# Kernel tuning notes

Measured on AMD Instinct MI355X. Metric: run time of the kernel, lower is better.

## Reference

```python
import jax, jax.numpy as jnp
import numpy as np

C, H, W = 3, 2048, 2048
N_ANN = 64
P = 512  # patch resolution
RESIZE_FRAC = 0.5  # deterministic midpoint of resize_range=(0.25, 0.75)
MIN_SIZE = 10


def setup_inputs() -> dict:
    key = jax.random.key(0)
    k1, k2, k3, k4 = jax.random.split(key, 4)
    image = jax.random.normal(k1, (C, H, W), jnp.float32)
    patch = jax.random.uniform(k2, (C, P, P), jnp.float32)
    # build valid normalized xyxy boxes (x1<x2, y1<y2) inside the image
    centers = jax.random.uniform(k3, (N_ANN, 2), minval=0.2, maxval=0.8)
    sizes = jax.random.uniform(k4, (N_ANN, 2), minval=0.10, maxval=0.30)
    xy1 = jnp.clip(centers - sizes / 2, 0.0, 1.0)
    xy2 = jnp.clip(centers + sizes / 2, 0.0, 1.0)
    annotations = jnp.concatenate([xy1, xy2], axis=1).astype(jnp.float32)  # [N,4] xyxy
    return {"image": image, "annotations": annotations, "patch": patch}


def reference(image, annotations, patch):
    """MODE_CENTER_BBOX forward: for each bbox, bilinearly resize the patch to
    wh x wh (wh = min(bbox_w, bbox_h) * RESIZE_FRAC, >= MIN_SIZE), then paste it
    centered in the bbox (clamped to the image). embed_patch's mask arithmetic
    (image_mask*image + patch_mask*patch) is exactly a region overwrite."""
    c, h, w = image.shape
    # normalized_annotations=True: scale by [W, H, W, H] then floor to long
    ann = np.asarray(annotations * jnp.array([w, h, w, h], jnp.float32)).astype(np.int64)
    img = image
    for x1, y1, x2, y2 in ann:
        bw, bh = int(x2 - x1), int(y2 - y1)
        wh = max(int(min(bw, bh) * RESIZE_FRAC), MIN_SIZE)
        rp = jax.image.resize(patch, (c, wh, wh), method="bilinear")
        x = int(x1) + bw // 2 - wh // 2
        y = int(y1) + bh // 2 - wh // 2
        y = max(min(h - wh, y), 0)
        x = max(min(w - wh, x), 0)
        img = img.at[:, y:y + wh, x:x + wh].set(rp)
    return img
```

## Files before the change

kernel.cpp:

```cpp
#include <hip/hip_runtime.h>

#define CCH 3
#define HH 2048
#define WW 2048
#define NANN 64
#define PSZ 512
#define HWIMG (HH * WW)
#define PP (PSZ * PSZ)
#define WHMAX 308
#define OYB 4
#define CHS ((size_t)PSZ * WHMAX)

__global__ void prep_kernel(const float* __restrict__ ann, int* __restrict__ meta) {
    int a = threadIdx.x;
    if (a >= NANN) return;
    float x1f = ann[a * 4 + 0] * (float)WW;
    float y1f = ann[a * 4 + 1] * (float)HH;
    float x2f = ann[a * 4 + 2] * (float)WW;
    float y2f = ann[a * 4 + 3] * (float)HH;
    int x1 = (int)x1f, y1 = (int)y1f, x2 = (int)x2f, y2 = (int)y2f;
    int bw = x2 - x1, bh = y2 - y1;
    int mn = bw < bh ? bw : bh;
    int wh = mn / 2;
    if (wh < 10) wh = 10;
    int x = x1 + bw / 2 - wh / 2;
    int y = y1 + bh / 2 - wh / 2;
    y = min(HH - wh, y); y = max(y, 0);
    x = min(WW - wh, x); x = max(x, 0);
    meta[a * 4 + 0] = x;
    meta[a * 4 + 1] = y;
    meta[a * 4 + 2] = wh;
    meta[a * 4 + 3] = 0;
}

__global__ __launch_bounds__(256) void resize_y4_kernel(
    const float* __restrict__ patch, const int* __restrict__ meta,
    float* __restrict__ tmp)
{
    const int a   = blockIdx.y;
    const int oy0 = blockIdx.x * OYB;
    const int wh  = meta[a * 4 + 2];
    if (oy0 >= wh) return;

    const int xx = threadIdx.x * 2;
    const float inv = 512.0f / (float)wh;
    const float rs  = (float)wh / 512.0f;

    float syf[OYB];
#pragma unroll
    for (int i = 0; i < OYB; ++i)
        syf[i] = ((float)(oy0 + i) + 0.5f) * inv - 0.5f;

    const int ylast = min(oy0 + OYB - 1, wh - 1);
    const float syfL = ((float)ylast + 0.5f) * inv - 0.5f;
    const int ylo = max(0,       (int)ceilf(syf[0] - inv));
    const int yhi = min(PSZ - 1, (int)floorf(syfL + inv));

    float2 ac[OYB][3];
    float dy[OYB];
#pragma unroll
    for (int i = 0; i < OYB; ++i) {
        dy[i] = 0.f;
#pragma unroll
        for (int c = 0; c < 3; ++c) { ac[i][c].x = 0.f; ac[i][c].y = 0.f; }
    }

    const float* p = patch + xx;
#pragma unroll 2
    for (int yy = ylo; yy <= yhi; ++yy) {
        const float* row = p + yy * PSZ;
        float2 v0 = *(const float2*)(row);
        float2 v1 = *(const float2*)(row + PP);
        float2 v2 = *(const float2*)(row + 2 * PP);
#pragma unroll
        for (int i = 0; i < OYB; ++i) {
            float w = fmaxf(0.f, 1.f - fabsf(syf[i] - (float)yy) * rs);
            dy[i] += w;
            ac[i][0].x = fmaf(w, v0.x, ac[i][0].x);
            ac[i][0].y = fmaf(w, v0.y, ac[i][0].y);
            ac[i][1].x = fmaf(w, v1.x, ac[i][1].x);
            ac[i][1].y = fmaf(w, v1.y, ac[i][1].y);
            ac[i][2].x = fmaf(w, v2.x, ac[i][2].x);
            ac[i][2].y = fmaf(w, v2.y, ac[i][2].y);
        }
    }

#pragma unroll
    for (int i = 0; i < OYB; ++i) {
        int oy = oy0 + i;
        if (oy < wh) {
            float s = 1.0f / dy[i];
            float* t = tmp + ((size_t)(a * 3) * WHMAX + oy) * PSZ + xx;
            float2 o0 = { ac[i][0].x * s, ac[i][0].y * s };
            float2 o1 = { ac[i][1].x * s, ac[i][1].y * s };
            float2 o2 = { ac[i][2].x * s, ac[i][2].y * s };
            *(float2*)(t)           = o0;
            *(float2*)(t + CHS)     = o1;
            *(float2*)(t + 2 * CHS) = o2;
        }
    }
}

__device__ __forceinline__ void resample_px(
    const float* __restrict__ tmp, int a, int wh, int jx, int jy,
    float& o0, float& o1, float& o2)
{
    const float inv = 512.0f / (float)wh;
    const float rs  = (float)wh / 512.0f;
    const float sxf = ((float)jx + 0.5f) * inv - 0.5f;
    const int xlo = max(0,       (int)ceilf(sxf - inv));
    const int xhi = min(PSZ - 1, (int)floorf(sxf + inv));

    int kstart = xlo & ~3;
    if (kstart > 496) kstart = 496;

    const float* tb = tmp + ((size_t)(a * 3) * WHMAX + jy) * PSZ;

    if (xhi - kstart <= 15) {
        float r0[16], r1[16], r2[16];
#pragma unroll
        for (int u = 0; u < 4; ++u) {
            float4 qa = *(const float4*)(tb + kstart + 4 * u);
            float4 qb = *(const float4*)(tb + CHS + kstart + 4 * u);
            float4 qc = *(const float4*)(tb + 2 * CHS + kstart + 4 * u);
            r0[4 * u + 0] = qa.x; r0[4 * u + 1] = qa.y; r0[4 * u + 2] = qa.z; r0[4 * u + 3] = qa.w;
            r1[4 * u + 0] = qb.x; r1[4 * u + 1] = qb.y; r1[4 * u + 2] = qb.z; r1[4 * u + 3] = qb.w;
            r2[4 * u + 0] = qc.x; r2[4 * u + 1] = qc.y; r2[4 * u + 2] = qc.z; r2[4 * u + 3] = qc.w;
        }
        float dx = 0.f, a0 = 0.f, a1 = 0.f, a2 = 0.f;
#pragma unroll
        for (int j = 0; j < 16; ++j) {
            int pos = kstart + j;
            float w = (pos <= xhi) ? fmaxf(0.f, 1.f - fabsf(sxf - (float)pos) * rs) : 0.f;
            dx += w;
            a0 = fmaf(w, r0[j], a0);
            a1 = fmaf(w, r1[j], a1);
            a2 = fmaf(w, r2[j], a2);
        }
        const float s = 1.0f / dx;
        o0 = a0 * s; o1 = a1 * s; o2 = a2 * s;
    } else {
        float dx = 0.f;
        for (int x = xlo; x <= xhi; ++x)
            dx += fmaxf(0.f, 1.f - fabsf(sxf - (float)x) * rs);
        float a0 = 0.f, a1 = 0.f, a2 = 0.f;
        for (int x = xlo; x <= xhi; ++x) {
            float w = fmaxf(0.f, 1.f - fabsf(sxf - (float)x) * rs);
            a0 = fmaf(w, tb[x],           a0);
            a1 = fmaf(w, tb[x + CHS],     a1);
            a2 = fmaf(w, tb[x + 2 * CHS], a2);
        }
        const float s = 1.0f / dx;
        o0 = a0 * s; o1 = a1 * s; o2 = a2 * s;
    }
}

__global__ __launch_bounds__(256) void composite4_kernel(
    const float* __restrict__ img, const float* __restrict__ tmp,
    const int* __restrict__ meta, float* __restrict__ out)
{
    __shared__ int sax[NANN], say[NANN], sawh[NANN];
    __shared__ unsigned long long smask;

    const int tid = threadIdx.x;
    const int bx = blockIdx.x * 256;
    const int by = blockIdx.y * 4;

    if (tid < NANN) {
        int x = meta[tid * 4 + 0];
        int y = meta[tid * 4 + 1];
        int wh = meta[tid * 4 + 2];
        sax[tid] = x; say[tid] = y; sawh[tid] = wh;
        bool ov = (x < bx + 256) && (x + wh > bx) && (y < by + 4) && (y + wh > by);
        unsigned long long mm = __ballot(ov);
        if (tid == 0) smask = mm;
    }
    __syncthreads();

    const int x0  = bx + (tid & 63) * 4;
    const int py  = by + (tid >> 6);
    const int idx = py * WW + x0;

    unsigned long long m = smask;
    if (m == 0) {
        *(float4*)(out + idx)             = *(const float4*)(img + idx);
        *(float4*)(out + idx + HWIMG)     = *(const float4*)(img + idx + HWIMG);
        *(float4*)(out + idx + 2 * HWIMG) = *(const float4*)(img + idx + 2 * HWIMG);
        return;
    }

    int h0 = -1, h1 = -1, h2 = -1, h3 = -1;
    int und = 0xF;
    while (m && und) {
        int a = 63 - __clzll(m); m &= ~(1ull << a);
        int ya = say[a], wha = sawh[a];
        if (py < ya || py >= ya + wha) continue;
        int xl = sax[a], xr = xl + wha;
        if ((und & 1) && x0     >= xl && x0     < xr) { h0 = a; und &= ~1; }
        if ((und & 2) && x0 + 1 >= xl && x0 + 1 < xr) { h1 = a; und &= ~2; }
        if ((und & 4) && x0 + 2 >= xl && x0 + 2 < xr) { h2 = a; und &= ~4; }
        if ((und & 8) && x0 + 3 >= xl && x0 + 3 < xr) { h3 = a; und &= ~8; }
    }

    float4 c0, c1, c2;
    if (und) {
        c0 = *(const float4*)(img + idx);
        c1 = *(const float4*)(img + idx + HWIMG);
        c2 = *(const float4*)(img + idx + 2 * HWIMG);
    }
    if (h0 >= 0) resample_px(tmp, h0, sawh[h0], x0     - sax[h0], py - say[h0], c0.x, c1.x, c2.x);
    if (h1 >= 0) resample_px(tmp, h1, sawh[h1], x0 + 1 - sax[h1], py - say[h1], c0.y, c1.y, c2.y);
    if (h2 >= 0) resample_px(tmp, h2, sawh[h2], x0 + 2 - sax[h2], py - say[h2], c0.z, c1.z, c2.z);
    if (h3 >= 0) resample_px(tmp, h3, sawh[h3], x0 + 3 - sax[h3], py - say[h3], c0.w, c1.w, c2.w);

    *(float4*)(out + idx)             = c0;
    *(float4*)(out + idx + HWIMG)     = c1;
    *(float4*)(out + idx + 2 * HWIMG) = c2;
}

extern "C" void kernel_launch(void* const* d_in, const int* in_sizes, int n_in,
                              void* d_out, int out_size, void* d_ws, size_t ws_size,
                              hipStream_t stream) {
    const float* img   = (const float*)d_in[0];
    const float* ann   = (const float*)d_in[1];
    const float* patch = (const float*)d_in[2];
    float* out = (float*)d_out;

    int*   meta = (int*)d_ws;
    float* tmp  = (float*)((char*)d_ws + 4096);

    hipLaunchKernelGGL(prep_kernel, dim3(1), dim3(64), 0, stream, ann, meta);
    hipLaunchKernelGGL(resize_y4_kernel, dim3((WHMAX + OYB - 1) / OYB, NANN), dim3(256),
                       0, stream, patch, meta, tmp);
    hipLaunchKernelGGL(composite4_kernel, dim3(WW / 256, HH / 4), dim3(256), 0, stream,
                       img, tmp, meta, out);
}
```

Measured before the change: 73.89 us.

## Precompute full resized patches in a separate x-resize kernel before compositing

Adds a resize_x kernel that finishes the horizontal resampling of every annotation patch into a compact per-annotation buffer. The composite kernel then reads final pixels directly instead of resampling on the fly for each covered pixel, which removes redundant per-pixel x-resampling and its divergent loads. The old path stays as a fallback when the workspace is too small. The cost is an extra kernel launch and an extra write and read of up to 64x3x308x308 floats. The weight computation is also reordered so the weights are computed before the loads.

```diff
diff --git a/kernel.cpp b/kernel.cpp
--- a/kernel.cpp
+++ b/kernel.cpp
@@ -10,6 +10,7 @@
 #define WHMAX 308
 #define OYB 4
 #define CHS ((size_t)PSZ * WHMAX)
+#define RPP ((size_t)WHMAX * WHMAX)
 
 __global__ void prep_kernel(const float* __restrict__ ann, int* __restrict__ meta) {
     int a = threadIdx.x;
@@ -101,44 +102,56 @@
     }
 }
 
-__device__ __forceinline__ void resample_px(
-    const float* __restrict__ tmp, int a, int wh, int jx, int jy,
-    float& o0, float& o1, float& o2)
+__global__ __launch_bounds__(256) void resize_x_kernel(
+    const float* __restrict__ tmp, const int* __restrict__ meta,
+    float* __restrict__ rp)
 {
+    const int a  = blockIdx.z;
+    const int oy = blockIdx.y;
+    const int wh = meta[a * 4 + 2];
+    if (oy >= wh) return;
+    const int ox = blockIdx.x * 256 + threadIdx.x;
+    if (ox >= wh) return;
+
     const float inv = 512.0f / (float)wh;
     const float rs  = (float)wh / 512.0f;
-    const float sxf = ((float)jx + 0.5f) * inv - 0.5f;
+    const float sxf = ((float)ox + 0.5f) * inv - 0.5f;
     const int xlo = max(0,       (int)ceilf(sxf - inv));
     const int xhi = min(PSZ - 1, (int)floorf(sxf + inv));
 
     int kstart = xlo & ~3;
     if (kstart > 496) kstart = 496;
 
-    const float* tb = tmp + ((size_t)(a * 3) * WHMAX + jy) * PSZ;
+    const float* tb = tmp + ((size_t)(a * 3) * WHMAX + oy) * PSZ;
+    const size_t ob = (size_t)(a * 3) * RPP + (size_t)oy * WHMAX + ox;
 
     if (xhi - kstart <= 15) {
-        float r0[16], r1[16], r2[16];
+        float wgt[16];
+        float dx = 0.f;
+#pragma unroll
+        for (int j = 0; j < 16; ++j) {
+            int pos = kstart + j;
+            float w = (pos <= xhi) ? fmaxf(0.f, 1.f - fabsf(sxf - (float)pos) * rs) : 0.f;
+            wgt[j] = w;
+            dx += w;
+        }
+        const float s = 1.0f / dx;
+        float a0 = 0.f, a1 = 0.f, a2 = 0.f;
 #pragma unroll
         for (int u = 0; u < 4; ++u) {
             float4 qa = *(const float4*)(tb + kstart + 4 * u);
             float4 qb = *(const float4*)(tb + CHS + kstart + 4 * u);
             float4 qc = *(const float4*)(tb + 2 * CHS + kstart + 4 * u);
-            r0[4 * u + 0] = qa.x; r0[4 * u + 1] = qa.y; r0[4 * u + 2] = qa.z; r0[4 * u + 3] = qa.w;
-            r1[4 * u + 0] = qb.x; r1[4 * u + 1] = qb.y; r1[4 * u + 2] = qb.z; r1[4 * u + 3] = qb.w;
-            r2[4 * u + 0] = qc.x; r2[4 * u + 1] = qc.y; r2[4 * u + 2] = qc.z; r2[4 * u + 3] = qc.w;
-        }
-        float dx = 0.f, a0 = 0.f, a1 = 0.f, a2 = 0.f;
-#pragma unroll
-        for (int j = 0; j < 16; ++j) {
-            int pos = kstart + j;
-            float w = (pos <= xhi) ? fmaxf(0.f, 1.f - fabsf(sxf - (float)pos) * rs) : 0.f;
-            dx += w;
-            a0 = fmaf(w, r0[j], a0);
-            a1 = fmaf(w, r1[j], a1);
-            a2 = fmaf(w, r2[j], a2);
-        }
-        const float s = 1.0f / dx;
-        o0 = a0 * s; o1 = a1 * s; o2 = a2 * s;
+            a0 = fmaf(wgt[4*u+0], qa.x, a0); a0 = fmaf(wgt[4*u+1], qa.y, a0);
+            a0 = fmaf(wgt[4*u+2], qa.z, a0); a0 = fmaf(wgt[4*u+3], qa.w, a0);
+            a1 = fmaf(wgt[4*u+0], qb.x, a1); a1 = fmaf(wgt[4*u+1], qb.y, a1);
+            a1 = fmaf(wgt[4*u+2], qb.z, a1); a1 = fmaf(wgt[4*u+3], qb.w, a1);
+            a2 = fmaf(wgt[4*u+0], qc.x, a2); a2 = fmaf(wgt[4*u+1], qc.y, a2);
+            a2 = fmaf(wgt[4*u+2], qc.z, a2); a2 = fmaf(wgt[4*u+3], qc.w, a2);
+        }
+        rp[ob]           = a0 * s;
+        rp[ob + RPP]     = a1 * s;
+        rp[ob + 2 * RPP] = a2 * s;
     } else {
         float dx = 0.f;
         for (int x = xlo; x <= xhi; ++x)
@@ -151,12 +164,62 @@
             a2 = fmaf(w, tb[x + 2 * CHS], a2);
         }
         const float s = 1.0f / dx;
-        o0 = a0 * s; o1 = a1 * s; o2 = a2 * s;
-    }
-}
-
+        rp[ob]           = a0 * s;
+        rp[ob + RPP]     = a1 * s;
+        rp[ob + 2 * RPP] = a2 * s;
+    }
+}
+
+__device__ __forceinline__ void resample_px(
+    const float* __restrict__ tmp, int a, int wh, int jx, int jy,
+    float& o0, float& o1, float& o2)
+{
+    const float inv = 512.0f / (float)wh;
+    const float rs  = (float)wh / 512.0f;
+    const float sxf = ((float)jx + 0.5f) * inv - 0.5f;
+    const int xlo = max(0,       (int)ceilf(sxf - inv));
+    const int xhi = min(PSZ - 1, (int)floorf(sxf + inv));
+    int kstart = xlo & ~3;
+    if (kstart > 496) kstart = 496;
+    const float* tb = tmp + ((size_t)(a * 3) * WHMAX + jy) * PSZ;
+    float dx = 0.f, a0 = 0.f, a1 = 0.f, a2 = 0.f;
+    if (xhi - kstart <= 15) {
+        float wgt[16];
+#pragma unroll
+        for (int j = 0; j < 16; ++j) {
+            int pos = kstart + j;
+            float w = (pos <= xhi) ? fmaxf(0.f, 1.f - fabsf(sxf - (float)pos) * rs) : 0.f;
+            wgt[j] = w; dx += w;
+        }
+#pragma unroll
+        for (int u = 0; u < 4; ++u) {
+            float4 qa = *(const float4*)(tb + kstart + 4 * u);
+            float4 qb = *(const float4*)(tb + CHS + kstart + 4 * u);
+            float4 qc = *(const float4*)(tb + 2 * CHS + kstart + 4 * u);
+            a0 = fmaf(wgt[4*u+0], qa.x, a0); a0 = fmaf(wgt[4*u+1], qa.y, a0);
+            a0 = fmaf(wgt[4*u+2], qa.z, a0); a0 = fmaf(wgt[4*u+3], qa.w, a0);
+            a1 = fmaf(wgt[4*u+0], qb.x, a1); a1 = fmaf(wgt[4*u+1], qb.y, a1);
+            a1 = fmaf(wgt[4*u+2], qb.z, a1); a1 = fmaf(wgt[4*u+3], qb.w, a1);
+            a2 = fmaf(wgt[4*u+0], qc.x, a2); a2 = fmaf(wgt[4*u+1], qc.y, a2);
+            a2 = fmaf(wgt[4*u+2], qc.z, a2); a2 = fmaf(wgt[4*u+3], qc.w, a2);
+        }
+    } else {
+        for (int x = xlo; x <= xhi; ++x)
+            dx += fmaxf(0.f, 1.f - fabsf(sxf - (float)x) * rs);
+        for (int x = xlo; x <= xhi; ++x) {
+            float w = fmaxf(0.f, 1.f - fabsf(sxf - (float)x) * rs);
+            a0 = fmaf(w, tb[x],           a0);
+            a1 = fmaf(w, tb[x + CHS],     a1);
+            a2 = fmaf(w, tb[x + 2 * CHS], a2);
+        }
+    }
+    const float s = 1.0f / dx;
+    o0 = a0 * s; o1 = a1 * s; o2 = a2 * s;
+}
+
+template <int USE_RP>
 __global__ __launch_bounds__(256) void composite4_kernel(
-    const float* __restrict__ img, const float* __restrict__ tmp,
+    const float* __restrict__ img, const float* __restrict__ src,
     const int* __restrict__ meta, float* __restrict__ out)
 {
     __shared__ int sax[NANN], say[NANN], sawh[NANN];
@@ -208,10 +271,18 @@
         c1 = *(const float4*)(img + idx + HWIMG);
         c2 = *(const float4*)(img + idx + 2 * HWIMG);
     }
-    if (h0 >= 0) resample_px(tmp, h0, sawh[h0], x0     - sax[h0], py - say[h0], c0.x, c1.x, c2.x);
-    if (h1 >= 0) resample_px(tmp, h1, sawh[h1], x0 + 1 - sax[h1], py - say[h1], c0.y, c1.y, c2.y);
-    if (h2 >= 0) resample_px(tmp, h2, sawh[h2], x0 + 2 - sax[h2], py - say[h2], c0.z, c1.z, c2.z);
-    if (h3 >= 0) resample_px(tmp, h3, sawh[h3], x0 + 3 - sax[h3], py - say[h3], c0.w, c1.w, c2.w);
+
+    if (USE_RP) {
+        if (h0 >= 0) { size_t b = (size_t)(h0*3)*RPP + (size_t)(py - say[h0])*WHMAX + (x0     - sax[h0]); c0.x = src[b]; c1.x = src[b + RPP]; c2.x = src[b + 2*RPP]; }
+        if (h1 >= 0) { size_t b = (size_t)(h1*3)*RPP + (size_t)(py - say[h1])*WHMAX + (x0 + 1 - sax[h1]); c0.y = src[b]; c1.y = src[b + RPP]; c2.y = src[b + 2*RPP]; }
+        if (h2 >= 0) { size_t b = (size_t)(h2*3)*RPP + (size_t)(py - say[h2])*WHMAX + (x0 + 2 - sax[h2]); c0.z = src[b]; c1.z = src[b + RPP]; c2.z = src[b + 2*RPP]; }
+        if (h3 >= 0) { size_t b = (size_t)(h3*3)*RPP + (size_t)(py - say[h3])*WHMAX + (x0 + 3 - sax[h3]); c0.w = src[b]; c1.w = src[b + RPP]; c2.w = src[b + 2*RPP]; }
+    } else {
+        if (h0 >= 0) resample_px(src, h0, sawh[h0], x0     - sax[h0], py - say[h0], c0.x, c1.x, c2.x);
+        if (h1 >= 0) resample_px(src, h1, sawh[h1], x0 + 1 - sax[h1], py - say[h1], c0.y, c1.y, c2.y);
+        if (h2 >= 0) resample_px(src, h2, sawh[h2], x0 + 2 - sax[h2], py - say[h2], c0.z, c1.z, c2.z);
+        if (h3 >= 0) resample_px(src, h3, sawh[h3], x0 + 3 - sax[h3], py - say[h3], c0.w, c1.w, c2.w);
+    }
 
     *(float4*)(out + idx)             = c0;
     *(float4*)(out + idx + HWIMG)     = c1;
@@ -228,10 +299,21 @@
 
     int*   meta = (int*)d_ws;
     float* tmp  = (float*)((char*)d_ws + 4096);
+    const size_t tmp_bytes = (size_t)NANN * 3 * WHMAX * PSZ * 4;
+    float* rp   = (float*)((char*)d_ws + 4096 + tmp_bytes);
+    const size_t need = 4096 + tmp_bytes + (size_t)NANN * 3 * WHMAX * WHMAX * 4;
 
     hipLaunchKernelGGL(prep_kernel, dim3(1), dim3(64), 0, stream, ann, meta);
     hipLaunchKernelGGL(resize_y4_kernel, dim3((WHMAX + OYB - 1) / OYB, NANN), dim3(256),
                        0, stream, patch, meta, tmp);
-    hipLaunchKernelGGL(composite4_kernel, dim3(WW / 256, HH / 4), dim3(256), 0, stream,
-                       img, tmp, meta, out);
-}
+
+    if (ws_size >= need) {
+        hipLaunchKernelGGL(resize_x_kernel, dim3(2, WHMAX, NANN), dim3(256), 0, stream,
+                           tmp, meta, rp);
+        hipLaunchKernelGGL((composite4_kernel<1>), dim3(WW / 256, HH / 4), dim3(256),
+                           0, stream, img, rp, meta, out);
+    } else {
+        hipLaunchKernelGGL((composite4_kernel<0>), dim3(WW / 256, HH / 4), dim3(256),
+                           0, stream, img, tmp, meta, out);
+    }
+}
```

Result: slower. 85.45 us (+15.6%).
